# Kernel optimization log

Hardware: AMD Instinct MI355X
Metric: run time of the kernel (lower is better)

Reference implementation:

```python
import jax, jax.numpy as jnp
from jax import lax
import numpy as np

T, N, C, D, K = 256, 4096, 12, 256, 12


def setup_inputs() -> dict:
    key = jax.random.key(0)
    ks = jax.random.split(key, 11)
    g = lambda k, shape: (jax.random.normal(k, shape, jnp.float32) * 0.05)
    return {
        "x": jax.random.normal(ks[0], (T, N, C), jnp.float32),
        "enc_Wx": g(ks[1], (D, C)),
        "enc_bx": g(ks[2], (D,)),
        "enc_Wh": g(ks[3], (D, D)),
        "enc_Wy": g(ks[4], (K, D)),
        "enc_by": g(ks[5], (K,)),
        "dec_Wx": g(ks[6], (D, C)),
        "dec_bx": g(ks[7], (D,)),
        "dec_Wh": g(ks[8], (D, D)),
        "dec_Wy": g(ks[9], (K, D)),
        "dec_by": g(ks[10], (K,)),
    }


def reference(x, enc_Wx, enc_bx, enc_Wh, enc_Wy, enc_by,
              dec_Wx, dec_bx, dec_Wh, dec_Wy, dec_by):
    # x: (T, N, C)
    Tn, Nn, Cn = x.shape
    Dn = enc_Wh.shape[0]

    # ---- encoder Elman RNN: h_t = relu(x2h(x_t) + h2h(h_{t-1})) ----
    # Precompute input projection for all timesteps (batched GEMM),
    # leaving only the D x D recurrence inside the scan.
    x_proj = jnp.einsum('tnc,dc->tnd', x, enc_Wx) + enc_bx  # (T, N, D)

    def enc_step(h, xp):
        h = jax.nn.relu(xp + h @ enc_Wh.T)
        return h, None

    h0 = jnp.zeros((Nn, Dn), x.dtype)
    h_last, _ = lax.scan(enc_step, h0, x_proj)  # (N, D) == enc_h[-1]
    # (encoder h2y output is computed in the original but discarded)

    # ---- decoder: greedy feedback loop, T steps ----
    sos0 = jnp.zeros((Nn, Cn), x.dtype).at[:, -2].set(1.0)

    def dec_step(carry, _):
        h, sos = carry
        h = jax.nn.relu(sos @ dec_Wx.T + dec_bx + h @ dec_Wh.T)  # (N, D)
        y = h @ dec_Wy.T + dec_by                                # (N, K)
        sos = jax.nn.one_hot(jnp.argmax(y, axis=-1), y.shape[-1],
                             dtype=x.dtype)                      # (N, C)
        return (h, sos), y

    _, ys = lax.scan(dec_step, (h_last, sos0), None, length=Tn)
    return ys  # (T, N, K)
```

## Files before the change

### kernel.cpp

```cpp
#include <hip/hip_runtime.h>
#include <cstdint>
#include <cstddef>

#define TT 256
#define NN 4096
#define CC 12
#define DD 256
#define KD 12
#define NB 16
#define NTH 512
#define HS 264
#define XS 40
#define YS 20

typedef _Float16 half8 __attribute__((ext_vector_type(8)));
typedef __fp16 fp16x2 __attribute__((ext_vector_type(2)));
typedef float f32x4 __attribute__((ext_vector_type(4)));
#define MFMA __builtin_amdgcn_mfma_f32_16x16x32_f16

struct FalseC { static constexpr bool value = false; };
struct TrueC  { static constexpr bool value = true;  };

struct alignas(16) SM {
  _Float16 hhi[2][NB][HS];
  _Float16 hlo[2][NB][HS];
  _Float16 xhi[4][NB][XS];
  _Float16 xlo[4][NB][XS];
  float    part2[2][8][NB][YS];
};

__device__ __forceinline__ void split8(const float* w, half8& hi, half8& lo) {
  #pragma unroll
  for (int j = 0; j < 8; ++j) {
    _Float16 h = (_Float16)w[j];
    hi[j] = h;
    lo[j] = (_Float16)(w[j] - (float)h);
  }
}

__device__ __forceinline__ void packpair(float v0, float v1,
                                         unsigned& hw, unsigned& lw) {
  union { fp16x2 v; unsigned u; } a, b;
  a.v = __builtin_amdgcn_cvt_pkrtz(v0, v1);
  const float r0 = (float)a.v[0], r1 = (float)a.v[1];
  b.v = __builtin_amdgcn_cvt_pkrtz(v0 - r0, v1 - r1);
  hw = a.u; lw = b.u;
}

__device__ __forceinline__ void BAR() {
  asm volatile("s_waitcnt lgkmcnt(0)" ::: "memory");
  __builtin_amdgcn_s_barrier();
  __builtin_amdgcn_sched_barrier(0);
}

__global__ __launch_bounds__(NTH, 2)
void seq2seq_kernel(const float* __restrict__ x,
                    const float* __restrict__ enc_Wx,
                    const float* __restrict__ enc_bx,
                    const float* __restrict__ enc_Wh,
                    const float* __restrict__ dec_Wx,
                    const float* __restrict__ dec_bx,
                    const float* __restrict__ dec_Wh,
                    const float* __restrict__ dec_Wy,
                    const float* __restrict__ dec_by,
                    float* __restrict__ out)
{
  __shared__ SM sm;
  const int tid  = (int)threadIdx.x;
  const int wid  = tid >> 6;
  const int lane = tid & 63;
  const int l15  = lane & 15;
  const int quad = lane >> 4;
  const int n0   = (int)blockIdx.x * NB;

  half8 Whi[2][8], Wlo[2][8];
  half8 Xhi[2], Xlo[2];
  float bxr[2];
  float pfA0 = 0.f, pfA1 = 0.f, pfA2 = 0.f;
  float pfB0 = 0.f, pfB1 = 0.f, pfB2 = 0.f;
  f32x4 accP[4], accQ[4];

  auto loadWh = [&](const float* __restrict__ W) {
    #pragma unroll
    for (int tt = 0; tt < 2; ++tt) {
      const int n = wid * 32 + 2 * l15 + tt;
      #pragma unroll
      for (int c = 0; c < 8; ++c) {
        float w[8];
        const float* p = W + (size_t)n * DD + c * 32 + quad * 8;
        *(float4*)&w[0] = *(const float4*)p;
        *(float4*)&w[4] = *(const float4*)(p + 4);
        split8(w, Whi[tt][c], Wlo[tt][c]);
      }
    }
  };
  auto loadWx = [&](const float* __restrict__ Wx) {
    #pragma unroll
    for (int tt = 0; tt < 2; ++tt) {
      const int n = wid * 32 + 2 * l15 + tt;
      float w[8];
      #pragma unroll
      for (int j = 0; j < 8; ++j) {
        const int k = quad * 8 + j;
        w[j] = (k < CC) ? Wx[(size_t)n * CC + k] : 0.f;
      }
      split8(w, Xhi[tt], Xlo[tt]);
    }
  };
  auto loadBx = [&](const float* __restrict__ bx) {
    #pragma unroll
    for (int tt = 0; tt < 2; ++tt) bxr[tt] = bx[wid * 32 + 2 * l15 + tt];
  };

  {
    unsigned* z;
    z = (unsigned*)&sm.hhi[0][0][0];
    for (int i = tid; i < NB * HS / 2; i += NTH) z[i] = 0u;
    z = (unsigned*)&sm.hlo[0][0][0];
    for (int i = tid; i < NB * HS / 2; i += NTH) z[i] = 0u;
    z = (unsigned*)&sm.xhi[0][0][0];
    for (int i = tid; i < 4 * NB * XS / 2; i += NTH) z[i] = 0u;
    z = (unsigned*)&sm.xlo[0][0][0];
    for (int i = tid; i < 4 * NB * XS / 2; i += NTH) z[i] = 0u;
  }
  loadWh(enc_Wh);
  loadWx(enc_Wx);
  loadBx(enc_bx);
  if (wid == 1) {
    const float* xg = x + ((size_t)2 * NN + n0) * CC;
    pfB0 = xg[lane]; pfB1 = xg[lane + 64]; pfB2 = xg[lane + 128];
  }
  BAR();
  #pragma unroll
  for (int s = 0; s < 2; ++s) {
    if (tid < NB * CC) {
      const float v = x[((size_t)s * NN + n0) * CC + tid];
      const _Float16 h = (_Float16)v;
      sm.xhi[s][tid / CC][tid % CC] = h;
      sm.xlo[s][tid / CC][tid % CC] = (_Float16)(v - (float)h);
    }
  }
  BAR();
  #pragma unroll
  for (int i = 0; i < 4; ++i) accP[i] = (f32x4){0.f, 0.f, 0.f, 0.f};
  {
    const half8 xh = *(const half8*)&sm.xhi[0][l15][quad * 8];
    const half8 xl = *(const half8*)&sm.xlo[0][l15][quad * 8];
    accP[0] = MFMA(xh, Xhi[0], accP[0], 0, 0, 0);
    accP[1] = MFMA(xh, Xhi[1], accP[1], 0, 0, 0);
    accP[2] = MFMA(xl, Xhi[0], accP[2], 0, 0, 0);
    accP[3] = MFMA(xl, Xhi[1], accP[3], 0, 0, 0);
    accP[2] = MFMA(xh, Xlo[0], accP[2], 0, 0, 0);
    accP[3] = MFMA(xh, Xlo[1], accP[3], 0, 0, 0);
  }

  auto encCore = [&](int t, f32x4 (&cur)[4], f32x4 (&nxt)[4],
                     float pw0, float pw1, float pw2) {
    const int rb = t & 1, wb = rb ^ 1;
    const _Float16* hh = &sm.hhi[rb][l15][0];
    const _Float16* hl = &sm.hlo[rb][l15][0];
    #pragma unroll
    for (int c = 0; c < 8; ++c) {
      const half8 ahi = *(const half8*)(hh + c * 32 + quad * 8);
      const half8 alo = *(const half8*)(hl + c * 32 + quad * 8);
      cur[0] = MFMA(ahi, Whi[0][c], cur[0], 0, 0, 0);
      cur[1] = MFMA(ahi, Whi[1][c], cur[1], 0, 0, 0);
      cur[2] = MFMA(alo, Whi[0][c], cur[2], 0, 0, 0);
      cur[3] = MFMA(alo, Whi[1][c], cur[3], 0, 0, 0);
      cur[0] = MFMA(ahi, Wlo[0][c], cur[0], 0, 0, 0);
      cur[1] = MFMA(ahi, Wlo[1][c], cur[1], 0, 0, 0);
    }
    #pragma unroll
    for (int i = 0; i < 4; ++i) nxt[i] = (f32x4){0.f, 0.f, 0.f, 0.f};
    if (t + 1 < TT) {
      const int xs = (t + 1) & 3;
      const half8 xh = *(const half8*)&sm.xhi[xs][l15][quad * 8];
      const half8 xl = *(const half8*)&sm.xlo[xs][l15][quad * 8];
      nxt[0] = MFMA(xh, Xhi[0], nxt[0], 0, 0, 0);
      nxt[1] = MFMA(xh, Xhi[1], nxt[1], 0, 0, 0);
      nxt[2] = MFMA(xl, Xhi[0], nxt[2], 0, 0, 0);
      nxt[3] = MFMA(xl, Xhi[1], nxt[3], 0, 0, 0);
      nxt[2] = MFMA(xh, Xlo[0], nxt[2], 0, 0, 0);
      nxt[3] = MFMA(xh, Xlo[1], nxt[3], 0, 0, 0);
    }
    const int colh = wid * 32 + 2 * l15;
    #pragma unroll
    for (int r = 0; r < 4; ++r) {
      const int m = quad * 4 + r;
      const float v0 = fmaxf(cur[0][r] + cur[2][r] + bxr[0], 0.f);
      const float v1 = fmaxf(cur[1][r] + cur[3][r] + bxr[1], 0.f);
      unsigned hw, lw;
      packpair(v0, v1, hw, lw);
      *(unsigned*)&sm.hhi[wb][m][colh] = hw;
      *(unsigned*)&sm.hlo[wb][m][colh] = lw;
    }
    if (wid == 1) {
      const int xw = (t + 2) & 3;
      #pragma unroll
      for (int j = 0; j < 3; ++j) {
        const int i = lane + 64 * j;
        const float vv = (j == 0) ? pw0 : (j == 1) ? pw1 : pw2;
        const _Float16 hx = (_Float16)vv;
        sm.xhi[xw][i / CC][i % CC] = hx;
        sm.xlo[xw][i / CC][i % CC] = (_Float16)(vv - (float)hx);
      }
    }
    BAR();
  };

  auto encBody = [&](int t, auto IAc) {
    constexpr bool IA = decltype(IAc)::value;
    if (wid == 1) {
      const int tp = (t + 3 < TT) ? (t + 3) : (TT - 1);
      const float* xg = x + ((size_t)tp * NN + n0) * CC;
      if constexpr (IA) { pfA0 = xg[lane]; pfA1 = xg[lane + 64]; pfA2 = xg[lane + 128]; }
      else              { pfB0 = xg[lane]; pfB1 = xg[lane + 64]; pfB2 = xg[lane + 128]; }
    }
    if constexpr (IA) encCore(t, accP, accQ, pfB0, pfB1, pfB2);
    else              encCore(t, accQ, accP, pfA0, pfA1, pfA2);
  };

  for (int t = 0; t < TT; t += 2) {
    encBody(t, TrueC{});
    encBody(t + 1, FalseC{});
  }

  loadWh(dec_Wh);
  loadWx(dec_Wx);
  loadBx(dec_bx);
  float by4[4];
  #pragma unroll
  for (int j = 0; j < 4; ++j) {
    const int o = quad * 4 + j;
    by4[j] = (o < KD) ? dec_by[o] : 0.f;
  }
  half8 wyh, wyl;
  {
    float w[8];
    if (l15 < KD) {
      const float* p = dec_Wy + (size_t)l15 * DD + wid * 32 + quad * 8;
      *(float4*)&w[0] = *(const float4*)p;
      *(float4*)&w[4] = *(const float4*)(p + 4);
    } else {
      #pragma unroll
      for (int j = 0; j < 8; ++j) w[j] = 0.f;
    }
    split8(w, wyh, wyl);
  }
  half8 aX;
  #pragma unroll
  for (int j = 0; j < 8; ++j)
    aX[j] = (_Float16)((quad * 8 + j == CC - 2) ? 1.f : 0.f);
  BAR();

  for (int t = 0; t < TT; ++t) {
    const int rb = t & 1, wb = rb ^ 1, pb = t & 1;
    f32x4 aA0 = {0.f,0.f,0.f,0.f}, aA1 = {0.f,0.f,0.f,0.f};
    f32x4 aB0 = {0.f,0.f,0.f,0.f}, aB1 = {0.f,0.f,0.f,0.f};
    aA0 = MFMA(aX, Xhi[0], aA0, 0, 0, 0);
    aA1 = MFMA(aX, Xhi[1], aA1, 0, 0, 0);
    aB0 = MFMA(aX, Xlo[0], aB0, 0, 0, 0);
    aB1 = MFMA(aX, Xlo[1], aB1, 0, 0, 0);
    const _Float16* hh = &sm.hhi[rb][l15][0];
    const _Float16* hl = &sm.hlo[rb][l15][0];
    #pragma unroll
    for (int c = 0; c < 8; ++c) {
      const half8 ahi = *(const half8*)(hh + c * 32 + quad * 8);
      const half8 alo = *(const half8*)(hl + c * 32 + quad * 8);
      aA0 = MFMA(ahi, Whi[0][c], aA0, 0, 0, 0);
      aA1 = MFMA(ahi, Whi[1][c], aA1, 0, 0, 0);
      aB0 = MFMA(alo, Whi[0][c], aB0, 0, 0, 0);
      aB1 = MFMA(alo, Whi[1][c], aB1, 0, 0, 0);
      aA0 = MFMA(ahi, Wlo[0][c], aA0, 0, 0, 0);
      aA1 = MFMA(ahi, Wlo[1][c], aA1, 0, 0, 0);
    }
    const int colh = wid * 32 + 2 * l15;
    #pragma unroll
    for (int r = 0; r < 4; ++r) {
      const int m = quad * 4 + r;
      const float v0 = fmaxf(aA0[r] + aB0[r] + bxr[0], 0.f);
      const float v1 = fmaxf(aA1[r] + aB1[r] + bxr[1], 0.f);
      unsigned hw, lw;
      packpair(v0, v1, hw, lw);
      *(unsigned*)&sm.hhi[wb][m][colh] = hw;
      *(unsigned*)&sm.hlo[wb][m][colh] = lw;
    }
    asm volatile("s_waitcnt lgkmcnt(0)" ::: "memory");
    const half8 yh8 = *(const half8*)&sm.hhi[wb][l15][wid * 32 + quad * 8];
    const half8 yl8 = *(const half8*)&sm.hlo[wb][l15][wid * 32 + quad * 8];
    f32x4 yp = {0.f,0.f,0.f,0.f};
    yp = MFMA(yh8, wyh, yp, 0, 0, 0);
    yp = MFMA(yl8, wyh, yp, 0, 0, 0);
    yp = MFMA(yh8, wyl, yp, 0, 0, 0);
    #pragma unroll
    for (int r = 0; r < 4; ++r)
      sm.part2[pb][wid][quad * 4 + r][l15] = yp[r];
    BAR();
    f32x4 ys = *(const f32x4*)&sm.part2[pb][0][l15][quad * 4];
    #pragma unroll
    for (int w = 1; w < 8; ++w)
      ys += *(const f32x4*)&sm.part2[pb][w][l15][quad * 4];
    float yv[4];
    #pragma unroll
    for (int j = 0; j < 4; ++j) yv[j] = ys[j] + by4[j];
    if (wid == 0 && quad < 3) {
      float4 st; st.x = yv[0]; st.y = yv[1]; st.z = yv[2]; st.w = yv[3];
      *(float4*)&out[((size_t)t * NN + n0 + l15) * KD + quad * 4] = st;
    }
    float v = -1e30f; int io = 0;
    #pragma unroll
    for (int j = 0; j < 4; ++j) {
      const int o = quad * 4 + j;
      const float cv = (o < KD) ? yv[j] : -1e30f;
      const bool take = cv > v;
      io = take ? o : io;
      v  = take ? cv : v;
    }
    #pragma unroll
    for (int d = 16; d < 64; d <<= 1) {
      const float ov = __shfl_xor(v, d);
      const int   oi = __shfl_xor(io, d);
      const bool take = (ov > v) || (ov == v && oi < io);
      v  = take ? ov : v;
      io = take ? oi : io;
    }
    #pragma unroll
    for (int j = 0; j < 8; ++j)
      aX[j] = (_Float16)((quad * 8 + j == io) ? 1.f : 0.f);
  }
}

extern "C" void kernel_launch(void* const* d_in, const int* in_sizes, int n_in,
                              void* d_out, int out_size, void* d_ws, size_t ws_size,
                              hipStream_t stream) {
  (void)in_sizes; (void)n_in; (void)d_ws; (void)ws_size; (void)out_size;
  const float* x      = (const float*)d_in[0];
  const float* enc_Wx = (const float*)d_in[1];
  const float* enc_bx = (const float*)d_in[2];
  const float* enc_Wh = (const float*)d_in[3];
  const float* dec_Wx = (const float*)d_in[6];
  const float* dec_bx = (const float*)d_in[7];
  const float* dec_Wh = (const float*)d_in[8];
  const float* dec_Wy = (const float*)d_in[9];
  const float* dec_by = (const float*)d_in[10];
  float* outp = (float*)d_out;

  seq2seq_kernel<<<NN / NB, NTH, 0, stream>>>(
      x, enc_Wx, enc_bx, enc_Wh, dec_Wx, dec_bx, dec_Wh, dec_Wy, dec_by, outp);
}
```

Measured before the change: 798.0 us.

## Compute decoder output redundantly per wave to remove cross-wave reduction barrier

Each wave now computes the full y = h·Wy projection from the h vector it already reads for the recurrence, fused into the same MFMA loop. The output and argmax for step t-1 are produced at the start of step t, which removes the part2 shared-memory partial sums and one of the two barriers per step. The trade-off is redundant MFMA work in every wave, eight more half8 Wy registers, and dropping the lo-part correction of Wy, which lowers precision of y slightly.

New measurement: 1.081 ms. 35.4% more time.

```diff
diff --git a/kernel.cpp b/kernel.cpp
--- a/kernel.cpp
+++ b/kernel.cpp
@@ -11,7 +11,6 @@
 #define NTH 512
 #define HS 264
 #define XS 40
-#define YS 20
 
 typedef _Float16 half8 __attribute__((ext_vector_type(8)));
 typedef __fp16 fp16x2 __attribute__((ext_vector_type(2)));
@@ -26,7 +25,6 @@
   _Float16 hlo[2][NB][HS];
   _Float16 xhi[4][NB][XS];
   _Float16 xlo[4][NB][XS];
-  float    part2[2][8][NB][YS];
 };
 
 __device__ __forceinline__ void split8(const float* w, half8& hi, half8& lo) {
@@ -228,39 +226,29 @@
   loadWh(dec_Wh);
   loadWx(dec_Wx);
   loadBx(dec_bx);
-  float by4[4];
+  const float byv = (l15 < KD) ? dec_by[l15] : 0.f;
+  half8 Wy8[8];
   #pragma unroll
-  for (int j = 0; j < 4; ++j) {
-    const int o = quad * 4 + j;
-    by4[j] = (o < KD) ? dec_by[o] : 0.f;
-  }
-  half8 wyh, wyl;
-  {
+  for (int c = 0; c < 8; ++c) {
     float w[8];
     if (l15 < KD) {
-      const float* p = dec_Wy + (size_t)l15 * DD + wid * 32 + quad * 8;
+      const float* p = dec_Wy + (size_t)l15 * DD + c * 32 + quad * 8;
       *(float4*)&w[0] = *(const float4*)p;
       *(float4*)&w[4] = *(const float4*)(p + 4);
     } else {
       #pragma unroll
       for (int j = 0; j < 8; ++j) w[j] = 0.f;
     }
-    split8(w, wyh, wyl);
-  }
-  half8 aX;
-  #pragma unroll
-  for (int j = 0; j < 8; ++j)
-    aX[j] = (_Float16)((quad * 8 + j == CC - 2) ? 1.f : 0.f);
+    #pragma unroll
+    for (int j = 0; j < 8; ++j) Wy8[c][j] = (_Float16)w[j];
+  }
   BAR();
 
   for (int t = 0; t < TT; ++t) {
-    const int rb = t & 1, wb = rb ^ 1, pb = t & 1;
+    const int rb = t & 1, wb = rb ^ 1;
     f32x4 aA0 = {0.f,0.f,0.f,0.f}, aA1 = {0.f,0.f,0.f,0.f};
     f32x4 aB0 = {0.f,0.f,0.f,0.f}, aB1 = {0.f,0.f,0.f,0.f};
-    aA0 = MFMA(aX, Xhi[0], aA0, 0, 0, 0);
-    aA1 = MFMA(aX, Xhi[1], aA1, 0, 0, 0);
-    aB0 = MFMA(aX, Xlo[0], aB0, 0, 0, 0);
-    aB1 = MFMA(aX, Xlo[1], aB1, 0, 0, 0);
+    f32x4 yac = {0.f,0.f,0.f,0.f};
     const _Float16* hh = &sm.hhi[rb][l15][0];
     const _Float16* hl = &sm.hlo[rb][l15][0];
     #pragma unroll
@@ -273,7 +261,49 @@
       aB1 = MFMA(alo, Whi[1][c], aB1, 0, 0, 0);
       aA0 = MFMA(ahi, Wlo[0][c], aA0, 0, 0, 0);
       aA1 = MFMA(ahi, Wlo[1][c], aA1, 0, 0, 0);
-    }
+      yac = MFMA(ahi, Wy8[c], yac, 0, 0, 0);
+      yac = MFMA(alo, Wy8[c], yac, 0, 0, 0);
+    }
+    int g;
+    if (t == 0) {
+      g = CC - 2;
+    } else {
+      float vr[4]; int ir[4];
+      #pragma unroll
+      for (int r = 0; r < 4; ++r) {
+        vr[r] = (l15 < KD) ? yac[r] + byv : -1e30f;
+        ir[r] = l15;
+      }
+      if (wid == 0 && l15 < KD) {
+        #pragma unroll
+        for (int r = 0; r < 4; ++r)
+          out[((size_t)(t - 1) * NN + n0 + quad * 4 + r) * KD + l15] =
+              yac[r] + byv;
+      }
+      #pragma unroll
+      for (int d = 1; d < 16; d <<= 1) {
+        #pragma unroll
+        for (int r = 0; r < 4; ++r) {
+          const float ov = __shfl_xor(vr[r], d);
+          const int   oi = __shfl_xor(ir[r], d);
+          const bool take = (ov > vr[r]) || (ov == vr[r] && oi < ir[r]);
+          vr[r] = take ? ov : vr[r];
+          ir[r] = take ? oi : ir[r];
+        }
+      }
+      const int rsel = l15 & 3;
+      const int gsel = rsel == 0 ? ir[0] : rsel == 1 ? ir[1]
+                     : rsel == 2 ? ir[2] : ir[3];
+      g = __shfl(gsel, ((l15 >> 2) << 4) | l15);
+    }
+    half8 aX;
+    #pragma unroll
+    for (int j = 0; j < 8; ++j)
+      aX[j] = (_Float16)((quad * 8 + j == g) ? 1.f : 0.f);
+    aA0 = MFMA(aX, Xhi[0], aA0, 0, 0, 0);
+    aA1 = MFMA(aX, Xhi[1], aA1, 0, 0, 0);
+    aB0 = MFMA(aX, Xlo[0], aB0, 0, 0, 0);
+    aB1 = MFMA(aX, Xlo[1], aB1, 0, 0, 0);
     const int colh = wid * 32 + 2 * l15;
     #pragma unroll
     for (int r = 0; r < 4; ++r) {
@@ -285,48 +315,25 @@
       *(unsigned*)&sm.hhi[wb][m][colh] = hw;
       *(unsigned*)&sm.hlo[wb][m][colh] = lw;
     }
-    asm volatile("s_waitcnt lgkmcnt(0)" ::: "memory");
-    const half8 yh8 = *(const half8*)&sm.hhi[wb][l15][wid * 32 + quad * 8];
-    const half8 yl8 = *(const half8*)&sm.hlo[wb][l15][wid * 32 + quad * 8];
-    f32x4 yp = {0.f,0.f,0.f,0.f};
-    yp = MFMA(yh8, wyh, yp, 0, 0, 0);
-    yp = MFMA(yl8, wyh, yp, 0, 0, 0);
-    yp = MFMA(yh8, wyl, yp, 0, 0, 0);
-    #pragma unroll
-    for (int r = 0; r < 4; ++r)
-      sm.part2[pb][wid][quad * 4 + r][l15] = yp[r];
     BAR();
-    f32x4 ys = *(const f32x4*)&sm.part2[pb][0][l15][quad * 4];
-    #pragma unroll
-    for (int w = 1; w < 8; ++w)
-      ys += *(const f32x4*)&sm.part2[pb][w][l15][quad * 4];
-    float yv[4];
-    #pragma unroll
-    for (int j = 0; j < 4; ++j) yv[j] = ys[j] + by4[j];
-    if (wid == 0 && quad < 3) {
-      float4 st; st.x = yv[0]; st.y = yv[1]; st.z = yv[2]; st.w = yv[3];
-      *(float4*)&out[((size_t)t * NN + n0 + l15) * KD + quad * 4] = st;
-    }
-    float v = -1e30f; int io = 0;
-    #pragma unroll
-    for (int j = 0; j < 4; ++j) {
-      const int o = quad * 4 + j;
-      const float cv = (o < KD) ? yv[j] : -1e30f;
-      const bool take = cv > v;
-      io = take ? o : io;
-      v  = take ? cv : v;
-    }
-    #pragma unroll
-    for (int d = 16; d < 64; d <<= 1) {
-      const float ov = __shfl_xor(v, d);
-      const int   oi = __shfl_xor(io, d);
-      const bool take = (ov > v) || (ov == v && oi < io);
-      v  = take ? ov : v;
-      io = take ? oi : io;
-    }
-    #pragma unroll
-    for (int j = 0; j < 8; ++j)
-      aX[j] = (_Float16)((quad * 8 + j == io) ? 1.f : 0.f);
+  }
+  {
+    f32x4 yac = {0.f,0.f,0.f,0.f};
+    const _Float16* hh = &sm.hhi[0][l15][0];
+    const _Float16* hl = &sm.hlo[0][l15][0];
+    #pragma unroll
+    for (int c = 0; c < 8; ++c) {
+      const half8 ahi = *(const half8*)(hh + c * 32 + quad * 8);
+      const half8 alo = *(const half8*)(hl + c * 32 + quad * 8);
+      yac = MFMA(ahi, Wy8[c], yac, 0, 0, 0);
+      yac = MFMA(alo, Wy8[c], yac, 0, 0, 0);
+    }
+    if (wid == 0 && l15 < KD) {
+      #pragma unroll
+      for (int r = 0; r < 4; ++r)
+        out[((size_t)(TT - 1) * NN + n0 + quad * 4 + r) * KD + l15] =
+            yac[r] + byv;
+    }
   }
 }
 
```
